# Optimization experiments

Measured on AMD Instinct MI355X. Metric: run time of the kernel, lower is better.

## Reference

```python
import jax, jax.numpy as jnp
import numpy as np

EMBED_DIM = 768
NUM_HEADS = 12
PROJ_DIM = EMBED_DIM // NUM_HEADS
B, S = 8, 512
PRIOR_VAR = 0.01
LOG_PRIOR_VAR = float(np.log(PRIOR_VAR))


def _kl_regularizer(w_mu, w_sigma):
    # kl_loss broadcasts [in,units] mu against [units] logvar, then mean over all
    kl_loss = (LOG_PRIOR_VAR - 1.0 - w_sigma
               + jnp.log1p(jnp.exp(w_sigma)) / PRIOR_VAR
               + jnp.square(w_mu) / PRIOR_VAR)
    return 0.5 * jnp.mean(kl_loss)


def _linear_not_first(mu_in, Sigma_in, w_mu, w_sigma):
    in_dim = jnp.float32(w_mu.shape[0])
    units = jnp.float32(w_mu.shape[1])
    x_dim = jnp.float32(mu_in.shape[-1])
    mu_out = mu_in @ w_mu
    kl = _kl_regularizer(w_mu, w_sigma)
    W_Sigma = jnp.log1p(jnp.exp(w_sigma))  # softplus, shape [units]
    # w_t_Sigma_i_w: (w_mu/sqrt(in_dim))^2 = w_mu^2/in_dim
    Sigma_1 = Sigma_in @ (jnp.square(w_mu) / in_dim)
    # x_Sigma_w_x_T: x/x_dim, then sum(x*x) * W_Sigma
    xs = mu_in / x_dim
    xx_t = jnp.sum(xs * xs, axis=-1, keepdims=True)
    Sigma_2 = xx_t * W_Sigma
    # tr_Sigma_w_Sigma_in
    Sigma_3 = jnp.sum(Sigma_in, axis=-1, keepdims=True) * W_Sigma / units
    Sigma_out = jax.nn.softplus(Sigma_1 + Sigma_2 + Sigma_3)
    return mu_out, Sigma_out, kl


def _separate_heads(x):
    # [B,S,E] -> [B,H,S,d]
    return x.reshape(B, S, NUM_HEADS, PROJ_DIM).transpose(0, 2, 1, 3)


def _attention(mu_q, sg_q, mu_k, sg_k, mu_v, sg_v):
    dk = jnp.float32(PROJ_DIM)
    mu_score = jnp.einsum('bhqd,bhkd->bhqk', mu_q, mu_k)
    a = jnp.einsum('bhqd,bhkd->bhqk', jnp.square(mu_q) / dk, sg_k)
    # NOTE: faithful to TF source: matmul(mu_key^2/dk, sigma_query, transpose_b)
    b = jnp.einsum('bhkd,bhqd->bhkq', jnp.square(mu_k) / dk, sg_q)
    c = jnp.einsum('bhqd,bhkd->bhqk', sg_q, sg_k) / dk
    sigma_score = a + b + c
    mu_scaled = mu_score / jnp.sqrt(dk)
    sigma_scaled = sigma_score / dk
    mu_w = jax.nn.softmax(mu_scaled, axis=-1)
    wd = jnp.float32(mu_w.shape[-1])
    grad = jnp.square(mu_w - jnp.square(mu_w))
    Sigma_w = grad * sigma_scaled / wd
    mu_out = jnp.einsum('bhqk,bhkd->bhqd', mu_w, mu_v)
    d = jnp.einsum('bhqk,bhkd->bhqd', jnp.square(mu_w) / wd, sg_v)
    e = jnp.einsum('bhqk,bhkd->bhqd', Sigma_w, jnp.square(mu_v) / wd)
    f = jnp.einsum('bhqk,bhkd->bhqd', Sigma_w, sg_v) / wd
    return mu_out, jax.nn.softplus(d + e + f)


def _forward(mu_inputs, sigma_inputs, wq_mu, wq_sigma, wk_mu, wk_sigma,
             wv_mu, wv_sigma, wo_mu, wo_sigma):
    # eval mode: VDP_Dropout is identity
    mu_q, sg_q, kl_q = _linear_not_first(mu_inputs, sigma_inputs, wq_mu, wq_sigma)
    mu_k, sg_k, kl_k = _linear_not_first(mu_inputs, sigma_inputs, wk_mu, wk_sigma)
    mu_v, sg_v, kl_v = _linear_not_first(mu_inputs, sigma_inputs, wv_mu, wv_sigma)
    mu_q, sg_q = _separate_heads(mu_q), _separate_heads(sg_q)
    mu_k, sg_k = _separate_heads(mu_k), _separate_heads(sg_k)
    mu_v, sg_v = _separate_heads(mu_v), _separate_heads(sg_v)
    mu_att, sg_att = _attention(mu_q, sg_q, mu_k, sg_k, mu_v, sg_v)
    mu_cat = mu_att.transpose(0, 2, 1, 3).reshape(B, S, EMBED_DIM)
    sg_cat = sg_att.transpose(0, 2, 1, 3).reshape(B, S, EMBED_DIM)
    mu_out, Sigma_out, kl_o = _linear_not_first(mu_cat, sg_cat, wo_mu, wo_sigma)
    kl = kl_q + kl_k + kl_v + kl_o
    return mu_out, Sigma_out, kl


def setup_inputs() -> dict:
    key = jax.random.key(0)
    ks = jax.random.split(key, 10)
    glorot = float(np.sqrt(2.0 / (EMBED_DIM + EMBED_DIM)))
    def w_pair(k1, k2):
        w_mu = jax.random.normal(k1, (EMBED_DIM, EMBED_DIM), jnp.float32) * glorot
        w_sigma = jax.random.uniform(k2, (EMBED_DIM,), jnp.float32,
                                     minval=-4.6, maxval=-2.25)
        return w_mu, w_sigma
    wq_mu, wq_sigma = w_pair(ks[0], ks[1])
    wk_mu, wk_sigma = w_pair(ks[2], ks[3])
    wv_mu, wv_sigma = w_pair(ks[4], ks[5])
    wo_mu, wo_sigma = w_pair(ks[6], ks[7])
    mu_inputs = jax.random.normal(ks[8], (B, S, EMBED_DIM), jnp.float32)
    sigma_inputs = jax.random.uniform(ks[9], (B, S, EMBED_DIM), jnp.float32)
    return {"mu_inputs": mu_inputs, "sigma_inputs": sigma_inputs,
            "wq_mu": wq_mu, "wq_sigma": wq_sigma,
            "wk_mu": wk_mu, "wk_sigma": wk_sigma,
            "wv_mu": wv_mu, "wv_sigma": wv_sigma,
            "wo_mu": wo_mu, "wo_sigma": wo_sigma}


def reference(mu_inputs, sigma_inputs, wq_mu, wq_sigma, wk_mu, wk_sigma,
              wv_mu, wv_sigma, wo_mu, wo_sigma):
    return _forward(mu_inputs, sigma_inputs, wq_mu, wq_sigma, wk_mu, wk_sigma,
                    wv_mu, wv_sigma, wo_mu, wo_sigma)
```

## Files before the change

kernel.cpp:

```cpp
#include <hip/hip_runtime.h>
#include <math.h>

constexpr int E = 768;
constexpr int H = 12;
constexpr int D = 64;
constexpr int Bsz = 8;
constexpr int S = 512;
constexpr int NROWS = Bsz * S;
constexpr int NE_ = NROWS * E;
constexpr int WE = E * E;
constexpr float LOG_PV_M1 = -5.605170185988091f;
constexpr float INV_PV = 100.0f;

typedef __attribute__((ext_vector_type(8))) short short8;
typedef __attribute__((ext_vector_type(4))) float floatx4;

__device__ __forceinline__ float softplusf(float x) {
    return fmaxf(x, 0.f) + log1pf(expf(-fabsf(x)));
}
__device__ __forceinline__ unsigned short f2bf(float f) {
    unsigned int u = __float_as_uint(f);
    unsigned int r = (u + 0x7fffu + ((u >> 16) & 1u)) >> 16;
    return (unsigned short)r;
}
__device__ __forceinline__ float bf2f(unsigned short h) {
    return __uint_as_float(((unsigned int)h) << 16);
}
__device__ __forceinline__ unsigned int pack2(float a, float b) {
    return (unsigned int)f2bf(a) | ((unsigned int)f2bf(b) << 16);
}

__global__ void zero_kernel(float* p) { if (threadIdx.x == 0) p[0] = 0.f; }

__global__ __launch_bounds__(256) void kl_kernel(const float* __restrict__ wmu,
                                                 const float* __restrict__ wsig,
                                                 float* __restrict__ out) {
    int tid = blockIdx.x * 256 + threadIdx.x;
    int nthr = gridDim.x * 256;
    float partial = 0.f;
    for (int i = tid; i < E * E; i += nthr) {
        float w = wmu[i];
        partial += w * w;
    }
    partial *= INV_PV;
    if (tid < E) {
        float ws = wsig[tid];
        partial += (float)E * (LOG_PV_M1 - ws + softplusf(ws) * INV_PV);
    }
    __shared__ float red[256];
    red[threadIdx.x] = partial;
    __syncthreads();
    for (int s = 128; s > 0; s >>= 1) {
        if (threadIdx.x < s) red[threadIdx.x] += red[threadIdx.x + s];
        __syncthreads();
    }
    if (threadIdx.x == 0)
        atomicAdd(out, 0.5f * red[0] / (float)(E * E));
}

__global__ __launch_bounds__(256) void pack_in_kernel(const float* __restrict__ mu,
                                                      const float* __restrict__ sg,
                                                      unsigned short* __restrict__ m16,
                                                      unsigned short* __restrict__ s16) {
    size_t i = ((size_t)blockIdx.x * 256 + threadIdx.x) * 8;
    float4 a0 = *(const float4*)(mu + i);
    float4 a1 = *(const float4*)(mu + i + 4);
    *(uint4*)(m16 + i) = make_uint4(pack2(a0.x, a0.y), pack2(a0.z, a0.w),
                                    pack2(a1.x, a1.y), pack2(a1.z, a1.w));
    float4 b0 = *(const float4*)(sg + i);
    float4 b1 = *(const float4*)(sg + i + 4);
    *(uint4*)(s16 + i) = make_uint4(pack2(b0.x, b0.y), pack2(b0.z, b0.w),
                                    pack2(b1.x, b1.y), pack2(b1.z, b1.w));
}

__global__ __launch_bounds__(256) void packT_kernel(
    const float* __restrict__ w0, const float* __restrict__ w1,
    const float* __restrict__ w2, const float* __restrict__ w3,
    unsigned short* __restrict__ wtm, unsigned short* __restrict__ wts) {
    const float* W = (blockIdx.z == 0) ? w0 : (blockIdx.z == 1) ? w1
                   : (blockIdx.z == 2) ? w2 : w3;
    unsigned short* om = wtm + (size_t)blockIdx.z * WE;
    unsigned short* os = wts + (size_t)blockIdx.z * WE;
    __shared__ float tile[32][33];
    int k0 = blockIdx.x * 32, n0 = blockIdx.y * 32;
    int t = threadIdx.x;
    {
        int r = t >> 3, c = (t & 7) * 4;
        float4 v = *(const float4*)&W[(size_t)(k0 + r) * E + n0 + c];
        tile[r][c] = v.x; tile[r][c + 1] = v.y; tile[r][c + 2] = v.z; tile[r][c + 3] = v.w;
    }
    __syncthreads();
    {
        int n = t >> 3, r = (t & 7) * 4;
        float v0 = tile[r][n], v1 = tile[r + 1][n], v2 = tile[r + 2][n], v3 = tile[r + 3][n];
        size_t o = (size_t)(n0 + n) * E + k0 + r;
        *(uint2*)&om[o] = make_uint2(pack2(v0, v1), pack2(v2, v3));
        const float is = 1.f / 768.f;
        *(uint2*)&os[o] = make_uint2(pack2(v0 * v0 * is, v1 * v1 * is),
                                     pack2(v2 * v2 * is, v3 * v3 * is));
    }
}

__global__ __launch_bounds__(256) void rowstats_kernel(const float* __restrict__ mu,
                                                       const float* __restrict__ sg,
                                                       float* __restrict__ xx,
                                                       float* __restrict__ ss) {
    int wave = threadIdx.x >> 6, lane = threadIdx.x & 63;
    int row = blockIdx.x * 4 + wave;
    const float* mrow = mu + (size_t)row * E;
    const float* srow = sg + (size_t)row * E;
    float s2 = 0.f, s1 = 0.f;
    for (int i = lane; i < E; i += 64) {
        float m = mrow[i];
        s2 += m * m;
        s1 += srow[i];
    }
    for (int off = 32; off > 0; off >>= 1) {
        s2 += __shfl_xor(s2, off);
        s1 += __shfl_xor(s1, off);
    }
    if (lane == 0) {
        xx[row] = s2 * (1.f / ((float)E * (float)E));
        ss[row] = s1;
    }
}

__global__ __launch_bounds__(256) void rowstats16_kernel(const unsigned short* __restrict__ m16,
                                                         const unsigned short* __restrict__ s16,
                                                         float* __restrict__ xx,
                                                         float* __restrict__ ss) {
    int wave = threadIdx.x >> 6, lane = threadIdx.x & 63;
    int row = blockIdx.x * 4 + wave;
    const unsigned short* mrow = m16 + (size_t)row * E;
    const unsigned short* srow = s16 + (size_t)row * E;
    float s2 = 0.f, s1 = 0.f;
    for (int c = lane; c < 96; c += 64) {
        uint4 um = *(const uint4*)(mrow + c * 8);
        uint4 us = *(const uint4*)(srow + c * 8);
        unsigned int mw[4] = {um.x, um.y, um.z, um.w};
        unsigned int sw[4] = {us.x, us.y, us.z, us.w};
#pragma unroll
        for (int j = 0; j < 4; ++j) {
            float a = bf2f((unsigned short)(mw[j] & 0xffff));
            float b = bf2f((unsigned short)(mw[j] >> 16));
            s2 += a * a + b * b;
            s1 += bf2f((unsigned short)(sw[j] & 0xffff)) + bf2f((unsigned short)(sw[j] >> 16));
        }
    }
    for (int off = 32; off > 0; off >>= 1) {
        s2 += __shfl_xor(s2, off);
        s1 += __shfl_xor(s1, off);
    }
    if (lane == 0) {
        xx[row] = s2 * (1.f / ((float)E * (float)E));
        ss[row] = s1;
    }
}

template <int ROLE>
__global__ __launch_bounds__(512, 1) void linear2_kernel(
    const unsigned short* __restrict__ A16m, const unsigned short* __restrict__ A16s,
    const unsigned short* __restrict__ WTm, const unsigned short* __restrict__ WTs,
    const float* __restrict__ wsig, const float* __restrict__ xx, const float* __restrict__ ss,
    void* __restrict__ o0v, void* __restrict__ o1v, void* __restrict__ o2v) {
    constexpr int LDK = 40;
    __shared__ unsigned short A_mu[64][LDK], A_sg[64][LDK];
    __shared__ unsigned short W_mu[128][LDK], W_sg[128][LDK];
    const int m0 = blockIdx.x * 64, n0 = blockIdx.y * 128;
    const int t = threadIdx.x, lane = t & 63, wid = t >> 6;
    const int qsub = wid >> 1, c2 = wid & 1;
    const int lr = lane & 15, lg = lane >> 4;

    floatx4 accm[4] = {{0.f,0.f,0.f,0.f},{0.f,0.f,0.f,0.f},{0.f,0.f,0.f,0.f},{0.f,0.f,0.f,0.f}};
    floatx4 accs[4] = {{0.f,0.f,0.f,0.f},{0.f,0.f,0.f,0.f},{0.f,0.f,0.f,0.f},{0.f,0.f,0.f,0.f}};

    for (int k0 = 0; k0 < E; k0 += 32) {
        __syncthreads();
        {
            int r = t >> 3, c = (t & 7) * 4;
            *(uint2*)&A_mu[r][c] = *(const uint2*)(A16m + (size_t)(m0 + r) * E + k0 + c);
            *(uint2*)&A_sg[r][c] = *(const uint2*)(A16s + (size_t)(m0 + r) * E + k0 + c);
        }
        {
            int n = t >> 2, c = (t & 3) * 8;
            *(uint4*)&W_mu[n][c] = *(const uint4*)(WTm + (size_t)(n0 + n) * E + k0 + c);
            *(uint4*)&W_sg[n][c] = *(const uint4*)(WTs + (size_t)(n0 + n) * E + k0 + c);
        }
        __syncthreads();
        short8 a_mu = *(const short8*)&A_mu[qsub * 16 + lr][lg * 8];
        short8 a_sg = *(const short8*)&A_sg[qsub * 16 + lr][lg * 8];
#pragma unroll
        for (int f = 0; f < 4; ++f) {
            int col = c2 * 64 + f * 16 + lr;
            short8 b_mu = *(const short8*)&W_mu[col][lg * 8];
            short8 b_sg = *(const short8*)&W_sg[col][lg * 8];
            accm[f] = __builtin_amdgcn_mfma_f32_16x16x32_bf16(a_mu, b_mu, accm[f], 0, 0, 0);
            accs[f] = __builtin_amdgcn_mfma_f32_16x16x32_bf16(a_sg, b_sg, accs[f], 0, 0, 0);
        }
    }
#pragma unroll
    for (int f = 0; f < 4; ++f) {
        int n = n0 + c2 * 64 + f * 16 + lr;
        float WS = softplusf(wsig[n]);
#pragma unroll
        for (int v = 0; v < 4; ++v) {
            int m = m0 + qsub * 16 + lg * 4 + v;
            size_t off = (size_t)m * E + n;
            float mu = accm[f][v];
            float sgo = softplusf(accs[f][v] + xx[m] * WS + ss[m] * WS * (1.f / 768.f));
            if (ROLE == 0) {
                unsigned short hi = f2bf(mu);
                ((unsigned short*)o0v)[off] = hi;
                ((unsigned short*)o1v)[off] = f2bf(mu - bf2f(hi));
                ((unsigned short*)o2v)[off] = f2bf(sgo);
            } else if (ROLE == 1) {
                ((unsigned short*)o0v)[off] = f2bf(mu);
                ((unsigned short*)o1v)[off] = f2bf(sgo);
                ((unsigned short*)o2v)[off] = f2bf(mu * mu + sgo);
            } else {
                ((float*)o0v)[off] = mu;
                ((float*)o1v)[off] = sgo;
            }
        }
    }
}

__global__ __launch_bounds__(512, 1) void attn2_kernel(
    const unsigned short* __restrict__ q_hi_g, const unsigned short* __restrict__ q_lo_g,
    const unsigned short* __restrict__ q_sg_g,
    const unsigned short* __restrict__ k_hi_g, const unsigned short* __restrict__ k_lo_g,
    const unsigned short* __restrict__ k_sg_g,
    const unsigned short* __restrict__ v_mu_g, const unsigned short* __restrict__ v_sg_g,
    const unsigned short* __restrict__ v_cb_g,
    unsigned short* __restrict__ a_m16, unsigned short* __restrict__ a_s16) {
    constexpr int QB = 64, KC = 64, LDK = 72;
    __shared__ unsigned short q_hi[QB][LDK], q_lo[QB][LDK], q_cb[QB][LDK], q_k2[QB][LDK];
    __shared__ unsigned short k_hi[KC][LDK], k_lo[KC][LDK], k_sg[KC][LDK], k_qsg[KC][LDK];
    __shared__ unsigned short vT_mu[D][LDK], vT_sg[D][LDK], vT_cb[D][LDK];
    __shared__ unsigned short p_w[QB][LDK], p_w2[QB][LDK], p_sw[QB][LDK];
    __shared__ float red_m[2][QB], red_z[2][QB];

    const int bid = blockIdx.x;
    const int qt = bid & 7;
    const int hb = bid >> 3;
    const int h = hb % H;
    const int b = hb / H;
    const int q0 = qt * QB;
    const int t = threadIdx.x;
    const int lane = t & 63, wid = t >> 6;
    const int qsub = wid >> 1, c2 = wid & 1;
    const int Q0 = qsub * 16;
    const int lr = lane & 15, lg = lane >> 4;
    const size_t base = (size_t)b * S * E + (size_t)h * D;

    {
        int r = t >> 3, g = (t & 7) * 8;
        size_t off = base + (size_t)(q0 + r) * E + g;
        uint4 hi4 = *(const uint4*)(q_hi_g + off);
        uint4 lo4 = *(const uint4*)(q_lo_g + off);
        uint4 sg4 = *(const uint4*)(q_sg_g + off);
        uint4 kh4 = *(const uint4*)(k_hi_g + off);
        uint4 kl4 = *(const uint4*)(k_lo_g + off);
        *(uint4*)&q_hi[r][g] = hi4;
        *(uint4*)&q_lo[r][g] = lo4;
        unsigned int hw[4] = {hi4.x, hi4.y, hi4.z, hi4.w};
        unsigned int lw[4] = {lo4.x, lo4.y, lo4.z, lo4.w};
        unsigned int sw[4] = {sg4.x, sg4.y, sg4.z, sg4.w};
        unsigned int khw[4] = {kh4.x, kh4.y, kh4.z, kh4.w};
        unsigned int klw[4] = {kl4.x, kl4.y, kl4.z, kl4.w};
        unsigned int cbw[4], k2w[4];
        const float i64 = 1.f / 64.f;
#pragma unroll
        for (int j = 0; j < 4; ++j) {
            float m0f = bf2f((unsigned short)(hw[j] & 0xffff)) + bf2f((unsigned short)(lw[j] & 0xffff));
            float m1f = bf2f((unsigned short)(hw[j] >> 16)) + bf2f((unsigned short)(lw[j] >> 16));
            float s0f = bf2f((unsigned short)(sw[j] & 0xffff));
            float s1f = bf2f((unsigned short)(sw[j] >> 16));
            cbw[j] = pack2((m0f * m0f + s0f) * i64, (m1f * m1f + s1f) * i64);
            float km0 = bf2f((unsigned short)(khw[j] & 0xffff)) + bf2f((unsigned short)(klw[j] & 0xffff));
            float km1 = bf2f((unsigned short)(khw[j] >> 16)) + bf2f((unsigned short)(klw[j] >> 16));
            k2w[j] = pack2(km0 * km0 * i64, km1 * km1 * i64);
        }
        *(uint4*)&q_cb[r][g] = make_uint4(cbw[0], cbw[1], cbw[2], cbw[3]);
        *(uint4*)&q_k2[r][g] = make_uint4(k2w[0], k2w[1], k2w[2], k2w[3]);
    }

    float mv[4], zv[4];
#pragma unroll
    for (int v = 0; v < 4; ++v) { mv[v] = -1e30f; zv[v] = 0.f; }

    for (int c = 0; c < S / KC; ++c) {
        __syncthreads();
        {
            int r = t >> 3, g = (t & 7) * 8;
            size_t off = base + (size_t)(c * KC + r) * E + g;
            *(uint4*)&k_hi[r][g] = *(const uint4*)(k_hi_g + off);
            *(uint4*)&k_lo[r][g] = *(const uint4*)(k_lo_g + off);
        }
        __syncthreads();
        floatx4 cm[2] = {{0.f, 0.f, 0.f, 0.f}, {0.f, 0.f, 0.f, 0.f}};
#pragma unroll
        for (int ks = 0; ks < 2; ++ks) {
            int ao = lg * 8 + ks * 32;
            short8 ahi = *(const short8*)&q_hi[Q0 + lr][ao];
            short8 alo = *(const short8*)&q_lo[Q0 + lr][ao];
#pragma unroll
            for (int f = 0; f < 2; ++f) {
                int key = c2 * 32 + f * 16 + lr;
                short8 bhi = *(const short8*)&k_hi[key][ao];
                short8 blo = *(const short8*)&k_lo[key][ao];
                cm[f] = __builtin_amdgcn_mfma_f32_16x16x32_bf16(ahi, bhi, cm[f], 0, 0, 0);
                cm[f] = __builtin_amdgcn_mfma_f32_16x16x32_bf16(ahi, blo, cm[f], 0, 0, 0);
                cm[f] = __builtin_amdgcn_mfma_f32_16x16x32_bf16(alo, bhi, cm[f], 0, 0, 0);
            }
        }
#pragma unroll
        for (int v = 0; v < 4; ++v) {
            float s0 = cm[0][v] * 0.125f, s1 = cm[1][v] * 0.125f;
            float cmx = fmaxf(s0, s1);
            for (int off = 1; off <= 8; off <<= 1) cmx = fmaxf(cmx, __shfl_xor(cmx, off));
            float ez = __expf(s0 - cmx) + __expf(s1 - cmx);
            for (int off = 1; off <= 8; off <<= 1) ez += __shfl_xor(ez, off);
            float nm = fmaxf(mv[v], cmx);
            zv[v] = zv[v] * __expf(mv[v] - nm) + ez * __expf(cmx - nm);
            mv[v] = nm;
        }
    }
    __syncthreads();
    if ((lane & 15) == 0) {
#pragma unroll
        for (int v = 0; v < 4; ++v) {
            int qr = Q0 + lg * 4 + v;
            red_m[c2][qr] = mv[v];
            red_z[c2][qr] = zv[v];
        }
    }
    __syncthreads();
    float fm[4], fzi[4];
#pragma unroll
    for (int v = 0; v < 4; ++v) {
        int qr = Q0 + lg * 4 + v;
        float m0 = red_m[0][qr], m1 = red_m[1][qr];
        float mm = fmaxf(m0, m1);
        float zz = red_z[0][qr] * __expf(m0 - mm) + red_z[1][qr] * __expf(m1 - mm);
        fm[v] = mm;
        fzi[v] = 1.f / zz;
    }

    floatx4 accm[2] = {{0.f, 0.f, 0.f, 0.f}, {0.f, 0.f, 0.f, 0.f}};
    floatx4 accs[2] = {{0.f, 0.f, 0.f, 0.f}, {0.f, 0.f, 0.f, 0.f}};
    for (int c = 0; c < S / KC; ++c) {
        __syncthreads();
        {
            int r = t >> 3, g = (t & 7) * 8;
            size_t off = base + (size_t)(c * KC + r) * E + g;
            *(uint4*)&k_hi[r][g] = *(const uint4*)(k_hi_g + off);
            *(uint4*)&k_lo[r][g] = *(const uint4*)(k_lo_g + off);
            *(uint4*)&k_sg[r][g] = *(const uint4*)(k_sg_g + off);
            *(uint4*)&k_qsg[r][g] = *(const uint4*)(q_sg_g + off);
        }
        {
            int kp = t & 31, dg = (t >> 5) * 4;
            size_t o0 = base + (size_t)(c * KC + 2 * kp) * E + dg;
            size_t o1 = o0 + E;
            uint2 am = *(const uint2*)(v_mu_g + o0), bm = *(const uint2*)(v_mu_g + o1);
            uint2 as_ = *(const uint2*)(v_sg_g + o0), bs_ = *(const uint2*)(v_sg_g + o1);
            uint2 ac = *(const uint2*)(v_cb_g + o0), bc = *(const uint2*)(v_cb_g + o1);
            *(unsigned int*)&vT_mu[dg + 0][2 * kp] = (am.x & 0xffffu) | (bm.x << 16);
            *(unsigned int*)&vT_mu[dg + 1][2 * kp] = (am.x >> 16) | (bm.x & 0xffff0000u);
            *(unsigned int*)&vT_mu[dg + 2][2 * kp] = (am.y & 0xffffu) | (bm.y << 16);
            *(unsigned int*)&vT_mu[dg + 3][2 * kp] = (am.y >> 16) | (bm.y & 0xffff0000u);
            *(unsigned int*)&vT_sg[dg + 0][2 * kp] = (as_.x & 0xffffu) | (bs_.x << 16);
            *(unsigned int*)&vT_sg[dg + 1][2 * kp] = (as_.x >> 16) | (bs_.x & 0xffff0000u);
            *(unsigned int*)&vT_sg[dg + 2][2 * kp] = (as_.y & 0xffffu) | (bs_.y << 16);
            *(unsigned int*)&vT_sg[dg + 3][2 * kp] = (as_.y >> 16) | (bs_.y & 0xffff0000u);
            *(unsigned int*)&vT_cb[dg + 0][2 * kp] = (ac.x & 0xffffu) | (bc.x << 16);
            *(unsigned int*)&vT_cb[dg + 1][2 * kp] = (ac.x >> 16) | (bc.x & 0xffff0000u);
            *(unsigned int*)&vT_cb[dg + 2][2 * kp] = (ac.y & 0xffffu) | (bc.y << 16);
            *(unsigned int*)&vT_cb[dg + 3][2 * kp] = (ac.y >> 16) | (bc.y & 0xffff0000u);
        }
        __syncthreads();
        floatx4 cm[2] = {{0.f, 0.f, 0.f, 0.f}, {0.f, 0.f, 0.f, 0.f}};
        floatx4 cs[2] = {{0.f, 0.f, 0.f, 0.f}, {0.f, 0.f, 0.f, 0.f}};
#pragma unroll
        for (int ks = 0; ks < 2; ++ks) {
            int ao = lg * 8 + ks * 32;
            short8 ahi = *(const short8*)&q_hi[Q0 + lr][ao];
            short8 alo = *(const short8*)&q_lo[Q0 + lr][ao];
            short8 acb = *(const short8*)&q_cb[Q0 + lr][ao];
            short8 ak2 = *(const short8*)&q_k2[Q0 + lr][ao];
#pragma unroll
            for (int f = 0; f < 2; ++f) {
                int key = c2 * 32 + f * 16 + lr;
                short8 bhi = *(const short8*)&k_hi[key][ao];
                short8 blo = *(const short8*)&k_lo[key][ao];
                short8 bsg = *(const short8*)&k_sg[key][ao];
                short8 bqs = *(const short8*)&k_qsg[key][ao];
                cm[f] = __builtin_amdgcn_mfma_f32_16x16x32_bf16(ahi, bhi, cm[f], 0, 0, 0);
                cm[f] = __builtin_amdgcn_mfma_f32_16x16x32_bf16(ahi, blo, cm[f], 0, 0, 0);
                cm[f] = __builtin_amdgcn_mfma_f32_16x16x32_bf16(alo, bhi, cm[f], 0, 0, 0);
                cs[f] = __builtin_amdgcn_mfma_f32_16x16x32_bf16(acb, bsg, cs[f], 0, 0, 0);
                cs[f] = __builtin_amdgcn_mfma_f32_16x16x32_bf16(ak2, bqs, cs[f], 0, 0, 0);
            }
        }
#pragma unroll
        for (int f = 0; f < 2; ++f)
#pragma unroll
            for (int v = 0; v < 4; ++v) {
                int qr = Q0 + lg * 4 + v;
                int key = c2 * 32 + f * 16 + lr;
                float w = __expf(cm[f][v] * 0.125f - fm[v]) * fzi[v];
                float sgs = cs[f][v] * (1.f / 64.f);
                float g1 = w - w * w;
                p_w[qr][key] = f2bf(w);
                p_w2[qr][key] = f2bf(w * w * (1.f / 512.f));
                p_sw[qr][key] = f2bf(g1 * g1 * sgs * (1.f / 262144.f));
            }
        __syncthreads();
#pragma unroll
        for (int ks = 0; ks < 2; ++ks) {
            int ko = lg * 8 + ks * 32;
            short8 aw = *(const short8*)&p_w[Q0 + lr][ko];
            short8 aw2 = *(const short8*)&p_w2[Q0 + lr][ko];
            short8 asw = *(const short8*)&p_sw[Q0 + lr][ko];
#pragma unroll
            for (int nf = 0; nf < 2; ++nf) {
                int dcol = (wid & 1) * 32 + nf * 16 + lr;
                short8 bvm = *(const short8*)&vT_mu[dcol][ko];
                short8 bvs = *(const short8*)&vT_sg[dcol][ko];
                short8 bvc = *(const short8*)&vT_cb[dcol][ko];
                accm[nf] = __builtin_amdgcn_mfma_f32_16x16x32_bf16(aw, bvm, accm[nf], 0, 0, 0);
                accs[nf] = __builtin_amdgcn_mfma_f32_16x16x32_bf16(aw2, bvs, accs[nf], 0, 0, 0);
                accs[nf] = __builtin_amdgcn_mfma_f32_16x16x32_bf16(asw, bvc, accs[nf], 0, 0, 0);
            }
        }
    }
#pragma unroll
    for (int nf = 0; nf < 2; ++nf)
#pragma unroll
        for (int v = 0; v < 4; ++v) {
            int qg = q0 + Q0 + lg * 4 + v;
            int dcol = (wid & 1) * 32 + nf * 16 + lr;
            size_t g = base + (size_t)qg * E + dcol;
            a_m16[g] = f2bf(accm[nf][v]);
            a_s16[g] = f2bf(softplusf(accs[nf][v]));
        }
}

extern "C" void kernel_launch(void* const* d_in, const int* in_sizes, int n_in,
                              void* d_out, int out_size, void* d_ws, size_t ws_size,
                              hipStream_t stream) {
    const float* mu_in = (const float*)d_in[0];
    const float* sg_in = (const float*)d_in[1];
    const float* wq_mu = (const float*)d_in[2];
    const float* wq_sg = (const float*)d_in[3];
    const float* wk_mu = (const float*)d_in[4];
    const float* wk_sg = (const float*)d_in[5];
    const float* wv_mu = (const float*)d_in[6];
    const float* wv_sg = (const float*)d_in[7];
    const float* wo_mu = (const float*)d_in[8];
    const float* wo_sg = (const float*)d_in[9];

    float* out_mu = (float*)d_out;
    float* out_sg = out_mu + (size_t)NE_;
    float* out_kl = out_sg + (size_t)NE_;

    unsigned short* sp = (unsigned short*)d_ws;
    unsigned short* in_m16 = sp;
    unsigned short* in_s16 = sp + (size_t)NE_;
    unsigned short* q_hi = sp + 2 * (size_t)NE_;
    unsigned short* q_lo = sp + 3 * (size_t)NE_;
    unsigned short* q_sg = sp + 4 * (size_t)NE_;
    unsigned short* k_hi = sp + 5 * (size_t)NE_;
    unsigned short* k_lo = sp + 6 * (size_t)NE_;
    unsigned short* k_sg = sp + 7 * (size_t)NE_;
    unsigned short* v_mu = sp + 8 * (size_t)NE_;
    unsigned short* v_sg = sp + 9 * (size_t)NE_;
    unsigned short* v_cb = sp + 10 * (size_t)NE_;
    unsigned short* a_m16 = sp + 11 * (size_t)NE_;
    unsigned short* a_s16 = sp + 12 * (size_t)NE_;
    unsigned short* wt_mu = sp + 13 * (size_t)NE_;
    unsigned short* wt_sg = wt_mu + 4 * (size_t)WE;
    float* fstats = (float*)(wt_sg + 4 * (size_t)WE);
    float* xx = fstats;
    float* ss = fstats + NROWS;
    float* xx2 = fstats + 2 * NROWS;
    float* ss2 = fstats + 3 * NROWS;

    zero_kernel<<<1, 64, 0, stream>>>(out_kl);
    kl_kernel<<<64, 256, 0, stream>>>(wq_mu, wq_sg, out_kl);
    kl_kernel<<<64, 256, 0, stream>>>(wk_mu, wk_sg, out_kl);
    kl_kernel<<<64, 256, 0, stream>>>(wv_mu, wv_sg, out_kl);
    kl_kernel<<<64, 256, 0, stream>>>(wo_mu, wo_sg, out_kl);

    pack_in_kernel<<<NE_ / 2048, 256, 0, stream>>>(mu_in, sg_in, in_m16, in_s16);
    packT_kernel<<<dim3(24, 24, 4), 256, 0, stream>>>(wq_mu, wk_mu, wv_mu, wo_mu, wt_mu, wt_sg);
    rowstats_kernel<<<NROWS / 4, 256, 0, stream>>>(mu_in, sg_in, xx, ss);

    dim3 ggrid(NROWS / 64, E / 128);
    linear2_kernel<0><<<ggrid, 512, 0, stream>>>(in_m16, in_s16, wt_mu, wt_sg,
                                                 wq_sg, xx, ss, q_hi, q_lo, q_sg);
    linear2_kernel<0><<<ggrid, 512, 0, stream>>>(in_m16, in_s16, wt_mu + (size_t)WE, wt_sg + (size_t)WE,
                                                 wk_sg, xx, ss, k_hi, k_lo, k_sg);
    linear2_kernel<1><<<ggrid, 512, 0, stream>>>(in_m16, in_s16, wt_mu + 2 * (size_t)WE, wt_sg + 2 * (size_t)WE,
                                                 wv_sg, xx, ss, v_mu, v_sg, v_cb);

    attn2_kernel<<<Bsz * H * (S / 64), 512, 0, stream>>>(q_hi, q_lo, q_sg, k_hi, k_lo, k_sg,
                                                         v_mu, v_sg, v_cb, a_m16, a_s16);

    rowstats16_kernel<<<NROWS / 4, 256, 0, stream>>>(a_m16, a_s16, xx2, ss2);
    linear2_kernel<2><<<ggrid, 512, 0, stream>>>(a_m16, a_s16, wt_mu + 3 * (size_t)WE, wt_sg + 3 * (size_t)WE,
                                                 wo_sg, xx2, ss2, out_mu, out_sg, nullptr);
}
```

Measured before the change: 514.0 us.

## Batch QKV projections into one launch and retile attention to 32-query blocks

The three Q/K/V projection GEMMs become one launch with a z-dimension selecting the weight and output role. The attention kernel is retiled to 32 queries per block, with eight waves arranged as 2 query slices by 4 key/dim slices. K, V and the transposed-V tiles now share one reused shared-memory buffer, which lowers LDS usage so two blocks can be resident per CU. Blocks are remapped across XCDs, and the softmax reduction merges four partials instead of two. The aim is better occupancy and fewer launches, at the cost of doubling the number of attention blocks, which each reload K/V per block, and adding an extra barrier per chunk.

```diff
diff --git a/kernel.cpp b/kernel.cpp
--- a/kernel.cpp
+++ b/kernel.cpp
@@ -157,12 +157,91 @@
     }
 }
 
-template <int ROLE>
-__global__ __launch_bounds__(512, 1) void linear2_kernel(
+__global__ __launch_bounds__(512, 1) void linear_qkv_kernel(
+    const unsigned short* __restrict__ A16m, const unsigned short* __restrict__ A16s,
+    const unsigned short* __restrict__ wt_mu, const unsigned short* __restrict__ wt_sg,
+    const float* __restrict__ wq_sig, const float* __restrict__ wk_sig,
+    const float* __restrict__ wv_sig,
+    const float* __restrict__ xx, const float* __restrict__ ss,
+    unsigned short* __restrict__ q_hi_g, unsigned short* __restrict__ q_lo_g,
+    unsigned short* __restrict__ q_sg_g,
+    unsigned short* __restrict__ k_hi_g, unsigned short* __restrict__ k_lo_g,
+    unsigned short* __restrict__ k_sg_g,
+    unsigned short* __restrict__ v_mu_g, unsigned short* __restrict__ v_sg_g,
+    unsigned short* __restrict__ v_cb_g) {
+    constexpr int LDK = 40;
+    __shared__ unsigned short A_mu[64][LDK], A_sg[64][LDK];
+    __shared__ unsigned short W_mu[128][LDK], W_sg[128][LDK];
+    const int z = blockIdx.z;
+    const unsigned short* WTm = wt_mu + (size_t)z * WE;
+    const unsigned short* WTs = wt_sg + (size_t)z * WE;
+    const float* wsig = (z == 0) ? wq_sig : (z == 1) ? wk_sig : wv_sig;
+    const int m0 = blockIdx.x * 64, n0 = blockIdx.y * 128;
+    const int t = threadIdx.x, lane = t & 63, wid = t >> 6;
+    const int qsub = wid >> 1, c2 = wid & 1;
+    const int lr = lane & 15, lg = lane >> 4;
+
+    floatx4 accm[4] = {{0.f,0.f,0.f,0.f},{0.f,0.f,0.f,0.f},{0.f,0.f,0.f,0.f},{0.f,0.f,0.f,0.f}};
+    floatx4 accs[4] = {{0.f,0.f,0.f,0.f},{0.f,0.f,0.f,0.f},{0.f,0.f,0.f,0.f},{0.f,0.f,0.f,0.f}};
+
+    for (int k0 = 0; k0 < E; k0 += 32) {
+        __syncthreads();
+        {
+            int r = t >> 3, c = (t & 7) * 4;
+            *(uint2*)&A_mu[r][c] = *(const uint2*)(A16m + (size_t)(m0 + r) * E + k0 + c);
+            *(uint2*)&A_sg[r][c] = *(const uint2*)(A16s + (size_t)(m0 + r) * E + k0 + c);
+        }
+        {
+            int n = t >> 2, c = (t & 3) * 8;
+            *(uint4*)&W_mu[n][c] = *(const uint4*)(WTm + (size_t)(n0 + n) * E + k0 + c);
+            *(uint4*)&W_sg[n][c] = *(const uint4*)(WTs + (size_t)(n0 + n) * E + k0 + c);
+        }
+        __syncthreads();
+        short8 a_mu = *(const short8*)&A_mu[qsub * 16 + lr][lg * 8];
+        short8 a_sg = *(const short8*)&A_sg[qsub * 16 + lr][lg * 8];
+#pragma unroll
+        for (int f = 0; f < 4; ++f) {
+            int col = c2 * 64 + f * 16 + lr;
+            short8 b_mu = *(const short8*)&W_mu[col][lg * 8];
+            short8 b_sg = *(const short8*)&W_sg[col][lg * 8];
+            accm[f] = __builtin_amdgcn_mfma_f32_16x16x32_bf16(a_mu, b_mu, accm[f], 0, 0, 0);
+            accs[f] = __builtin_amdgcn_mfma_f32_16x16x32_bf16(a_sg, b_sg, accs[f], 0, 0, 0);
+        }
+    }
+#pragma unroll
+    for (int f = 0; f < 4; ++f) {
+        int n = n0 + c2 * 64 + f * 16 + lr;
+        float WS = softplusf(wsig[n]);
+#pragma unroll
+        for (int v = 0; v < 4; ++v) {
+            int m = m0 + qsub * 16 + lg * 4 + v;
+            size_t off = (size_t)m * E + n;
+            float mu = accm[f][v];
+            float sgo = softplusf(accs[f][v] + xx[m] * WS + ss[m] * WS * (1.f / 768.f));
+            if (z == 0) {
+                unsigned short hi = f2bf(mu);
+                q_hi_g[off] = hi;
+                q_lo_g[off] = f2bf(mu - bf2f(hi));
+                q_sg_g[off] = f2bf(sgo);
+            } else if (z == 1) {
+                unsigned short hi = f2bf(mu);
+                k_hi_g[off] = hi;
+                k_lo_g[off] = f2bf(mu - bf2f(hi));
+                k_sg_g[off] = f2bf(sgo);
+            } else {
+                v_mu_g[off] = f2bf(mu);
+                v_sg_g[off] = f2bf(sgo);
+                v_cb_g[off] = f2bf(mu * mu + sgo);
+            }
+        }
+    }
+}
+
+__global__ __launch_bounds__(512, 1) void linear_out_kernel(
     const unsigned short* __restrict__ A16m, const unsigned short* __restrict__ A16s,
     const unsigned short* __restrict__ WTm, const unsigned short* __restrict__ WTs,
     const float* __restrict__ wsig, const float* __restrict__ xx, const float* __restrict__ ss,
-    void* __restrict__ o0v, void* __restrict__ o1v, void* __restrict__ o2v) {
+    float* __restrict__ Cmu, float* __restrict__ Csg) {
     constexpr int LDK = 40;
     __shared__ unsigned short A_mu[64][LDK], A_sg[64][LDK];
     __shared__ unsigned short W_mu[128][LDK], W_sg[128][LDK];
@@ -206,26 +285,13 @@
         for (int v = 0; v < 4; ++v) {
             int m = m0 + qsub * 16 + lg * 4 + v;
             size_t off = (size_t)m * E + n;
-            float mu = accm[f][v];
-            float sgo = softplusf(accs[f][v] + xx[m] * WS + ss[m] * WS * (1.f / 768.f));
-            if (ROLE == 0) {
-                unsigned short hi = f2bf(mu);
-                ((unsigned short*)o0v)[off] = hi;
-                ((unsigned short*)o1v)[off] = f2bf(mu - bf2f(hi));
-                ((unsigned short*)o2v)[off] = f2bf(sgo);
-            } else if (ROLE == 1) {
-                ((unsigned short*)o0v)[off] = f2bf(mu);
-                ((unsigned short*)o1v)[off] = f2bf(sgo);
-                ((unsigned short*)o2v)[off] = f2bf(mu * mu + sgo);
-            } else {
-                ((float*)o0v)[off] = mu;
-                ((float*)o1v)[off] = sgo;
-            }
-        }
-    }
-}
-
-__global__ __launch_bounds__(512, 1) void attn2_kernel(
+            Cmu[off] = accm[f][v];
+            Csg[off] = softplusf(accs[f][v] + xx[m] * WS + ss[m] * WS * (1.f / 768.f));
+        }
+    }
+}
+
+__global__ __launch_bounds__(512, 2) void attn3_kernel(
     const unsigned short* __restrict__ q_hi_g, const unsigned short* __restrict__ q_lo_g,
     const unsigned short* __restrict__ q_sg_g,
     const unsigned short* __restrict__ k_hi_g, const unsigned short* __restrict__ k_lo_g,
@@ -233,45 +299,43 @@
     const unsigned short* __restrict__ v_mu_g, const unsigned short* __restrict__ v_sg_g,
     const unsigned short* __restrict__ v_cb_g,
     unsigned short* __restrict__ a_m16, unsigned short* __restrict__ a_s16) {
-    constexpr int QB = 64, KC = 64, LDK = 72;
+    constexpr int QB = 32, KC = 64, LDK = 72;
     __shared__ unsigned short q_hi[QB][LDK], q_lo[QB][LDK], q_cb[QB][LDK], q_k2[QB][LDK];
-    __shared__ unsigned short k_hi[KC][LDK], k_lo[KC][LDK], k_sg[KC][LDK], k_qsg[KC][LDK];
-    __shared__ unsigned short vT_mu[D][LDK], vT_sg[D][LDK], vT_cb[D][LDK];
     __shared__ unsigned short p_w[QB][LDK], p_w2[QB][LDK], p_sw[QB][LDK];
-    __shared__ float red_m[2][QB], red_z[2][QB];
-
-    const int bid = blockIdx.x;
-    const int qt = bid & 7;
-    const int hb = bid >> 3;
+    __shared__ unsigned short uni[4][KC][LDK];
+    __shared__ float red_m[4][QB], red_z[4][QB];
+
+    const int p = blockIdx.x;
+    const int L = (p & 7) * 192 + (p >> 3);
+    const int qt = L & 15;
+    const int hb = L >> 4;
     const int h = hb % H;
     const int b = hb / H;
     const int q0 = qt * QB;
     const int t = threadIdx.x;
     const int lane = t & 63, wid = t >> 6;
-    const int qsub = wid >> 1, c2 = wid & 1;
+    const int qsub = wid >> 2, kq = wid & 3;
     const int Q0 = qsub * 16;
     const int lr = lane & 15, lg = lane >> 4;
     const size_t base = (size_t)b * S * E + (size_t)h * D;
 
     {
-        int r = t >> 3, g = (t & 7) * 8;
+        int r = t >> 4, g = (t & 15) * 4;
         size_t off = base + (size_t)(q0 + r) * E + g;
-        uint4 hi4 = *(const uint4*)(q_hi_g + off);
-        uint4 lo4 = *(const uint4*)(q_lo_g + off);
-        uint4 sg4 = *(const uint4*)(q_sg_g + off);
-        uint4 kh4 = *(const uint4*)(k_hi_g + off);
-        uint4 kl4 = *(const uint4*)(k_lo_g + off);
-        *(uint4*)&q_hi[r][g] = hi4;
-        *(uint4*)&q_lo[r][g] = lo4;
-        unsigned int hw[4] = {hi4.x, hi4.y, hi4.z, hi4.w};
-        unsigned int lw[4] = {lo4.x, lo4.y, lo4.z, lo4.w};
-        unsigned int sw[4] = {sg4.x, sg4.y, sg4.z, sg4.w};
-        unsigned int khw[4] = {kh4.x, kh4.y, kh4.z, kh4.w};
-        unsigned int klw[4] = {kl4.x, kl4.y, kl4.z, kl4.w};
-        unsigned int cbw[4], k2w[4];
+        uint2 hi2 = *(const uint2*)(q_hi_g + off);
+        uint2 lo2 = *(const uint2*)(q_lo_g + off);
+        uint2 sg2 = *(const uint2*)(q_sg_g + off);
+        uint2 kh2 = *(const uint2*)(k_hi_g + off);
+        uint2 kl2 = *(const uint2*)(k_lo_g + off);
+        *(uint2*)&q_hi[r][g] = hi2;
+        *(uint2*)&q_lo[r][g] = lo2;
+        unsigned int hw[2] = {hi2.x, hi2.y}, lw[2] = {lo2.x, lo2.y};
+        unsigned int sw[2] = {sg2.x, sg2.y};
+        unsigned int khw[2] = {kh2.x, kh2.y}, klw[2] = {kl2.x, kl2.y};
+        unsigned int cbw[2], k2w[2];
         const float i64 = 1.f / 64.f;
 #pragma unroll
-        for (int j = 0; j < 4; ++j) {
+        for (int j = 0; j < 2; ++j) {
             float m0f = bf2f((unsigned short)(hw[j] & 0xffff)) + bf2f((unsigned short)(lw[j] & 0xffff));
             float m1f = bf2f((unsigned short)(hw[j] >> 16)) + bf2f((unsigned short)(lw[j] >> 16));
             float s0f = bf2f((unsigned short)(sw[j] & 0xffff));
@@ -281,8 +345,8 @@
             float km1 = bf2f((unsigned short)(khw[j] >> 16)) + bf2f((unsigned short)(klw[j] >> 16));
             k2w[j] = pack2(km0 * km0 * i64, km1 * km1 * i64);
         }
-        *(uint4*)&q_cb[r][g] = make_uint4(cbw[0], cbw[1], cbw[2], cbw[3]);
-        *(uint4*)&q_k2[r][g] = make_uint4(k2w[0], k2w[1], k2w[2], k2w[3]);
+        *(uint2*)&q_cb[r][g] = make_uint2(cbw[0], cbw[1]);
+        *(uint2*)&q_k2[r][g] = make_uint2(k2w[0], k2w[1]);
     }
 
     float mv[4], zv[4];
@@ -294,32 +358,29 @@
         {
             int r = t >> 3, g = (t & 7) * 8;
             size_t off = base + (size_t)(c * KC + r) * E + g;
-            *(uint4*)&k_hi[r][g] = *(const uint4*)(k_hi_g + off);
-            *(uint4*)&k_lo[r][g] = *(const uint4*)(k_lo_g + off);
-        }
-        __syncthreads();
-        floatx4 cm[2] = {{0.f, 0.f, 0.f, 0.f}, {0.f, 0.f, 0.f, 0.f}};
+            *(uint4*)&uni[0][r][g] = *(const uint4*)(k_hi_g + off);
+            *(uint4*)&uni[1][r][g] = *(const uint4*)(k_lo_g + off);
+        }
+        __syncthreads();
+        floatx4 cm = {0.f, 0.f, 0.f, 0.f};
 #pragma unroll
         for (int ks = 0; ks < 2; ++ks) {
             int ao = lg * 8 + ks * 32;
             short8 ahi = *(const short8*)&q_hi[Q0 + lr][ao];
             short8 alo = *(const short8*)&q_lo[Q0 + lr][ao];
-#pragma unroll
-            for (int f = 0; f < 2; ++f) {
-                int key = c2 * 32 + f * 16 + lr;
-                short8 bhi = *(const short8*)&k_hi[key][ao];
-                short8 blo = *(const short8*)&k_lo[key][ao];
-                cm[f] = __builtin_amdgcn_mfma_f32_16x16x32_bf16(ahi, bhi, cm[f], 0, 0, 0);
-                cm[f] = __builtin_amdgcn_mfma_f32_16x16x32_bf16(ahi, blo, cm[f], 0, 0, 0);
-                cm[f] = __builtin_amdgcn_mfma_f32_16x16x32_bf16(alo, bhi, cm[f], 0, 0, 0);
-            }
+            int key = kq * 16 + lr;
+            short8 bhi = *(const short8*)&uni[0][key][ao];
+            short8 blo = *(const short8*)&uni[1][key][ao];
+            cm = __builtin_amdgcn_mfma_f32_16x16x32_bf16(ahi, bhi, cm, 0, 0, 0);
+            cm = __builtin_amdgcn_mfma_f32_16x16x32_bf16(ahi, blo, cm, 0, 0, 0);
+            cm = __builtin_amdgcn_mfma_f32_16x16x32_bf16(alo, bhi, cm, 0, 0, 0);
         }
 #pragma unroll
         for (int v = 0; v < 4; ++v) {
-            float s0 = cm[0][v] * 0.125f, s1 = cm[1][v] * 0.125f;
-            float cmx = fmaxf(s0, s1);
+            float s = cm[v] * 0.125f;
+            float cmx = s;
             for (int off = 1; off <= 8; off <<= 1) cmx = fmaxf(cmx, __shfl_xor(cmx, off));
-            float ez = __expf(s0 - cmx) + __expf(s1 - cmx);
+            float ez = __expf(s - cmx);
             for (int off = 1; off <= 8; off <<= 1) ez += __shfl_xor(ez, off);
             float nm = fmaxf(mv[v], cmx);
             zv[v] = zv[v] * __expf(mv[v] - nm) + ez * __expf(cmx - nm);
@@ -327,12 +388,12 @@
         }
     }
     __syncthreads();
-    if ((lane & 15) == 0) {
+    if (lr == 0) {
 #pragma unroll
         for (int v = 0; v < 4; ++v) {
             int qr = Q0 + lg * 4 + v;
-            red_m[c2][qr] = mv[v];
-            red_z[c2][qr] = zv[v];
+            red_m[kq][qr] = mv[v];
+            red_z[kq][qr] = zv[v];
         }
     }
     __syncthreads();
@@ -340,25 +401,62 @@
 #pragma unroll
     for (int v = 0; v < 4; ++v) {
         int qr = Q0 + lg * 4 + v;
-        float m0 = red_m[0][qr], m1 = red_m[1][qr];
-        float mm = fmaxf(m0, m1);
-        float zz = red_z[0][qr] * __expf(m0 - mm) + red_z[1][qr] * __expf(m1 - mm);
+        float m01 = fmaxf(red_m[0][qr], red_m[1][qr]);
+        float m23 = fmaxf(red_m[2][qr], red_m[3][qr]);
+        float mm = fmaxf(m01, m23);
+        float zz = red_z[0][qr] * __expf(red_m[0][qr] - mm)
+                 + red_z[1][qr] * __expf(red_m[1][qr] - mm)
+                 + red_z[2][qr] * __expf(red_m[2][qr] - mm)
+                 + red_z[3][qr] * __expf(red_m[3][qr] - mm);
         fm[v] = mm;
         fzi[v] = 1.f / zz;
     }
 
-    floatx4 accm[2] = {{0.f, 0.f, 0.f, 0.f}, {0.f, 0.f, 0.f, 0.f}};
-    floatx4 accs[2] = {{0.f, 0.f, 0.f, 0.f}, {0.f, 0.f, 0.f, 0.f}};
+    floatx4 accm = {0.f, 0.f, 0.f, 0.f};
+    floatx4 accs = {0.f, 0.f, 0.f, 0.f};
     for (int c = 0; c < S / KC; ++c) {
         __syncthreads();
         {
             int r = t >> 3, g = (t & 7) * 8;
             size_t off = base + (size_t)(c * KC + r) * E + g;
-            *(uint4*)&k_hi[r][g] = *(const uint4*)(k_hi_g + off);
-            *(uint4*)&k_lo[r][g] = *(const uint4*)(k_lo_g + off);
-            *(uint4*)&k_sg[r][g] = *(const uint4*)(k_sg_g + off);
-            *(uint4*)&k_qsg[r][g] = *(const uint4*)(q_sg_g + off);
-        }
+            *(uint4*)&uni[0][r][g] = *(const uint4*)(k_hi_g + off);
+            *(uint4*)&uni[1][r][g] = *(const uint4*)(k_lo_g + off);
+            *(uint4*)&uni[2][r][g] = *(const uint4*)(k_sg_g + off);
+            *(uint4*)&uni[3][r][g] = *(const uint4*)(q_sg_g + off);
+        }
+        __syncthreads();
+        floatx4 cm = {0.f, 0.f, 0.f, 0.f};
+        floatx4 cs = {0.f, 0.f, 0.f, 0.f};
+#pragma unroll
+        for (int ks = 0; ks < 2; ++ks) {
+            int ao = lg * 8 + ks * 32;
+            short8 ahi = *(const short8*)&q_hi[Q0 + lr][ao];
+            short8 alo = *(const short8*)&q_lo[Q0 + lr][ao];
+            short8 acb = *(const short8*)&q_cb[Q0 + lr][ao];
+            short8 ak2 = *(const short8*)&q_k2[Q0 + lr][ao];
+            int key = kq * 16 + lr;
+            short8 bhi = *(const short8*)&uni[0][key][ao];
+            short8 blo = *(const short8*)&uni[1][key][ao];
+            short8 bsg = *(const short8*)&uni[2][key][ao];
+            short8 bqs = *(const short8*)&uni[3][key][ao];
+            cm = __builtin_amdgcn_mfma_f32_16x16x32_bf16(ahi, bhi, cm, 0, 0, 0);
+            cm = __builtin_amdgcn_mfma_f32_16x16x32_bf16(ahi, blo, cm, 0, 0, 0);
+            cm = __builtin_amdgcn_mfma_f32_16x16x32_bf16(alo, bhi, cm, 0, 0, 0);
+            cs = __builtin_amdgcn_mfma_f32_16x16x32_bf16(acb, bsg, cs, 0, 0, 0);
+            cs = __builtin_amdgcn_mfma_f32_16x16x32_bf16(ak2, bqs, cs, 0, 0, 0);
+        }
+#pragma unroll
+        for (int v = 0; v < 4; ++v) {
+            int qr = Q0 + lg * 4 + v;
+            int key = kq * 16 + lr;
+            float w = __expf(cm[v] * 0.125f - fm[v]) * fzi[v];
+            float sgs = cs[v] * (1.f / 64.f);
+            float g1 = w - w * w;
+            p_w[qr][key] = f2bf(w);
+            p_w2[qr][key] = f2bf(w * w * (1.f / 512.f));
+            p_sw[qr][key] = f2bf(g1 * g1 * sgs * (1.f / 262144.f));
+        }
+        __syncthreads();
         {
             int kp = t & 31, dg = (t >> 5) * 4;
             size_t o0 = base + (size_t)(c * KC + 2 * kp) * E + dg;
@@ -366,56 +464,19 @@
             uint2 am = *(const uint2*)(v_mu_g + o0), bm = *(const uint2*)(v_mu_g + o1);
             uint2 as_ = *(const uint2*)(v_sg_g + o0), bs_ = *(const uint2*)(v_sg_g + o1);
             uint2 ac = *(const uint2*)(v_cb_g + o0), bc = *(const uint2*)(v_cb_g + o1);
-            *(unsigned int*)&vT_mu[dg + 0][2 * kp] = (am.x & 0xffffu) | (bm.x << 16);
-            *(unsigned int*)&vT_mu[dg + 1][2 * kp] = (am.x >> 16) | (bm.x & 0xffff0000u);
-            *(unsigned int*)&vT_mu[dg + 2][2 * kp] = (am.y & 0xffffu) | (bm.y << 16);
-            *(unsigned int*)&vT_mu[dg + 3][2 * kp] = (am.y >> 16) | (bm.y & 0xffff0000u);
-            *(unsigned int*)&vT_sg[dg + 0][2 * kp] = (as_.x & 0xffffu) | (bs_.x << 16);
-            *(unsigned int*)&vT_sg[dg + 1][2 * kp] = (as_.x >> 16) | (bs_.x & 0xffff0000u);
-            *(unsigned int*)&vT_sg[dg + 2][2 * kp] = (as_.y & 0xffffu) | (bs_.y << 16);
-            *(unsigned int*)&vT_sg[dg + 3][2 * kp] = (as_.y >> 16) | (bs_.y & 0xffff0000u);
-            *(unsigned int*)&vT_cb[dg + 0][2 * kp] = (ac.x & 0xffffu) | (bc.x << 16);
-            *(unsigned int*)&vT_cb[dg + 1][2 * kp] = (ac.x >> 16) | (bc.x & 0xffff0000u);
-            *(unsigned int*)&vT_cb[dg + 2][2 * kp] = (ac.y & 0xffffu) | (bc.y << 16);
-            *(unsigned int*)&vT_cb[dg + 3][2 * kp] = (ac.y >> 16) | (bc.y & 0xffff0000u);
-        }
-        __syncthreads();
-        floatx4 cm[2] = {{0.f, 0.f, 0.f, 0.f}, {0.f, 0.f, 0.f, 0.f}};
-        floatx4 cs[2] = {{0.f, 0.f, 0.f, 0.f}, {0.f, 0.f, 0.f, 0.f}};
-#pragma unroll
-        for (int ks = 0; ks < 2; ++ks) {
-            int ao = lg * 8 + ks * 32;
-            short8 ahi = *(const short8*)&q_hi[Q0 + lr][ao];
-            short8 alo = *(const short8*)&q_lo[Q0 + lr][ao];
-            short8 acb = *(const short8*)&q_cb[Q0 + lr][ao];
-            short8 ak2 = *(const short8*)&q_k2[Q0 + lr][ao];
-#pragma unroll
-            for (int f = 0; f < 2; ++f) {
-                int key = c2 * 32 + f * 16 + lr;
-                short8 bhi = *(const short8*)&k_hi[key][ao];
-                short8 blo = *(const short8*)&k_lo[key][ao];
-                short8 bsg = *(const short8*)&k_sg[key][ao];
-                short8 bqs = *(const short8*)&k_qsg[key][ao];
-                cm[f] = __builtin_amdgcn_mfma_f32_16x16x32_bf16(ahi, bhi, cm[f], 0, 0, 0);
-                cm[f] = __builtin_amdgcn_mfma_f32_16x16x32_bf16(ahi, blo, cm[f], 0, 0, 0);
-                cm[f] = __builtin_amdgcn_mfma_f32_16x16x32_bf16(alo, bhi, cm[f], 0, 0, 0);
-                cs[f] = __builtin_amdgcn_mfma_f32_16x16x32_bf16(acb, bsg, cs[f], 0, 0, 0);
-                cs[f] = __builtin_amdgcn_mfma_f32_16x16x32_bf16(ak2, bqs, cs[f], 0, 0, 0);
-            }
-        }
-#pragma unroll
-        for (int f = 0; f < 2; ++f)
-#pragma unroll
-            for (int v = 0; v < 4; ++v) {
-                int qr = Q0 + lg * 4 + v;
-                int key = c2 * 32 + f * 16 + lr;
-                float w = __expf(cm[f][v] * 0.125f - fm[v]) * fzi[v];
-                float sgs = cs[f][v] * (1.f / 64.f);
-                float g1 = w - w * w;
-                p_w[qr][key] = f2bf(w);
-                p_w2[qr][key] = f2bf(w * w * (1.f / 512.f));
-                p_sw[qr][key] = f2bf(g1 * g1 * sgs * (1.f / 262144.f));
-            }
+            *(unsigned int*)&uni[0][dg + 0][2 * kp] = (am.x & 0xffffu) | (bm.x << 16);
+            *(unsigned int*)&uni[0][dg + 1][2 * kp] = (am.x >> 16) | (bm.x & 0xffff0000u);
+            *(unsigned int*)&uni[0][dg + 2][2 * kp] = (am.y & 0xffffu) | (bm.y << 16);
+            *(unsigned int*)&uni[0][dg + 3][2 * kp] = (am.y >> 16) | (bm.y & 0xffff0000u);
+            *(unsigned int*)&uni[1][dg + 0][2 * kp] = (as_.x & 0xffffu) | (bs_.x << 16);
+            *(unsigned int*)&uni[1][dg + 1][2 * kp] = (as_.x >> 16) | (bs_.x & 0xffff0000u);
+            *(unsigned int*)&uni[1][dg + 2][2 * kp] = (as_.y & 0xffffu) | (bs_.y << 16);
+            *(unsigned int*)&uni[1][dg + 3][2 * kp] = (as_.y >> 16) | (bs_.y & 0xffff0000u);
+            *(unsigned int*)&uni[2][dg + 0][2 * kp] = (ac.x & 0xffffu) | (bc.x << 16);
+            *(unsigned int*)&uni[2][dg + 1][2 * kp] = (ac.x >> 16) | (bc.x & 0xffff0000u);
+            *(unsigned int*)&uni[2][dg + 2][2 * kp] = (ac.y & 0xffffu) | (bc.y << 16);
+            *(unsigned int*)&uni[2][dg + 3][2 * kp] = (ac.y >> 16) | (bc.y & 0xffff0000u);
+        }
         __syncthreads();
 #pragma unroll
         for (int ks = 0; ks < 2; ++ks) {
@@ -423,28 +484,23 @@
             short8 aw = *(const short8*)&p_w[Q0 + lr][ko];
             short8 aw2 = *(const short8*)&p_w2[Q0 + lr][ko];
             short8 asw = *(const short8*)&p_sw[Q0 + lr][ko];
-#pragma unroll
-            for (int nf = 0; nf < 2; ++nf) {
-                int dcol = (wid & 1) * 32 + nf * 16 + lr;
-                short8 bvm = *(const short8*)&vT_mu[dcol][ko];
-                short8 bvs = *(const short8*)&vT_sg[dcol][ko];
-                short8 bvc = *(const short8*)&vT_cb[dcol][ko];
-                accm[nf] = __builtin_amdgcn_mfma_f32_16x16x32_bf16(aw, bvm, accm[nf], 0, 0, 0);
-                accs[nf] = __builtin_amdgcn_mfma_f32_16x16x32_bf16(aw2, bvs, accs[nf], 0, 0, 0);
-                accs[nf] = __builtin_amdgcn_mfma_f32_16x16x32_bf16(asw, bvc, accs[nf], 0, 0, 0);
-            }
-        }
-    }
-#pragma unroll
-    for (int nf = 0; nf < 2; ++nf)
-#pragma unroll
-        for (int v = 0; v < 4; ++v) {
-            int qg = q0 + Q0 + lg * 4 + v;
-            int dcol = (wid & 1) * 32 + nf * 16 + lr;
-            size_t g = base + (size_t)qg * E + dcol;
-            a_m16[g] = f2bf(accm[nf][v]);
-            a_s16[g] = f2bf(softplusf(accs[nf][v]));
-        }
+            int dcol = kq * 16 + lr;
+            short8 bvm = *(const short8*)&uni[0][dcol][ko];
+            short8 bvs = *(const short8*)&uni[1][dcol][ko];
+            short8 bvc = *(const short8*)&uni[2][dcol][ko];
+            accm = __builtin_amdgcn_mfma_f32_16x16x32_bf16(aw, bvm, accm, 0, 0, 0);
+            accs = __builtin_amdgcn_mfma_f32_16x16x32_bf16(aw2, bvs, accs, 0, 0, 0);
+            accs = __builtin_amdgcn_mfma_f32_16x16x32_bf16(asw, bvc, accs, 0, 0, 0);
+        }
+    }
+#pragma unroll
+    for (int v = 0; v < 4; ++v) {
+        int qg = q0 + Q0 + lg * 4 + v;
+        int dcol = kq * 16 + lr;
+        size_t g = base + (size_t)qg * E + dcol;
+        a_m16[g] = f2bf(accm[v]);
+        a_s16[g] = f2bf(softplusf(accs[v]));
+    }
 }
 
 extern "C" void kernel_launch(void* const* d_in, const int* in_sizes, int n_in,
@@ -497,18 +553,15 @@
     packT_kernel<<<dim3(24, 24, 4), 256, 0, stream>>>(wq_mu, wk_mu, wv_mu, wo_mu, wt_mu, wt_sg);
     rowstats_kernel<<<NROWS / 4, 256, 0, stream>>>(mu_in, sg_in, xx, ss);
 
-    dim3 ggrid(NROWS / 64, E / 128);
-    linear2_kernel<0><<<ggrid, 512, 0, stream>>>(in_m16, in_s16, wt_mu, wt_sg,
-                                                 wq_sg, xx, ss, q_hi, q_lo, q_sg);
-    linear2_kernel<0><<<ggrid, 512, 0, stream>>>(in_m16, in_s16, wt_mu + (size_t)WE, wt_sg + (size_t)WE,
-                                                 wk_sg, xx, ss, k_hi, k_lo, k_sg);
-    linear2_kernel<1><<<ggrid, 512, 0, stream>>>(in_m16, in_s16, wt_mu + 2 * (size_t)WE, wt_sg + 2 * (size_t)WE,
-                                                 wv_sg, xx, ss, v_mu, v_sg, v_cb);
-
-    attn2_kernel<<<Bsz * H * (S / 64), 512, 0, stream>>>(q_hi, q_lo, q_sg, k_hi, k_lo, k_sg,
+    linear_qkv_kernel<<<dim3(NROWS / 64, E / 128, 3), 512, 0, stream>>>(
+        in_m16, in_s16, wt_mu, wt_sg, wq_sg, wk_sg, wv_sg, xx, ss,
+        q_hi, q_lo, q_sg, k_hi, k_lo, k_sg, v_mu, v_sg, v_cb);
+
+    attn3_kernel<<<Bsz * H * (S / 32), 512, 0, stream>>>(q_hi, q_lo, q_sg, k_hi, k_lo, k_sg,
                                                          v_mu, v_sg, v_cb, a_m16, a_s16);
 
     rowstats16_kernel<<<NROWS / 4, 256, 0, stream>>>(a_m16, a_s16, xx2, ss2);
-    linear2_kernel<2><<<ggrid, 512, 0, stream>>>(a_m16, a_s16, wt_mu + 3 * (size_t)WE, wt_sg + 3 * (size_t)WE,
-                                                 wo_sg, xx2, ss2, out_mu, out_sg, nullptr);
-}
+    linear_out_kernel<<<dim3(NROWS / 64, E / 128), 512, 0, stream>>>(
+        a_m16, a_s16, wt_mu + 3 * (size_t)WE, wt_sg + 3 * (size_t)WE,
+        wo_sg, xx2, ss2, out_mu, out_sg);
+}
```

New measurement: 495.0 us. -3.7%, faster.
